# Kernel tuning notes

Hardware: AMD Instinct MI355X
Metric: run time of the kernel (lower is better)

Reference implementation:

```python
import jax, jax.numpy as jnp
import numpy as np

K, PS, WS, WT = 7, 7, 8, 1
NHEADS, STRIDE0, STRIDE1 = 2, 4, 1


def reflect(idx, n):
    # mirror (no edge repeat) reflection, as in stnls reflect_bounds
    idx = jnp.where(idx < 0, -idx, idx)
    idx = jnp.where(idx >= n, 2 * (n - 1) - idx, idx)
    return idx


def setup_inputs():
    key = jax.random.key(0)
    k0, k1 = jax.random.split(key)
    B, T, C, H, W = 1, 4, 64, 192, 192
    vid0 = jax.random.normal(k0, (B, T, C, H, W), jnp.float32)
    vid1 = jax.random.normal(k1, (B, T, C, H, W), jnp.float32)
    return {"vid0": vid0, "vid1": vid1}


def _search(vid0, vid1):
    B, T, C, H, W = vid0.shape
    m = NHEADS
    cph = C // m
    psh = PS // 2
    nH, nW = H // STRIDE0, W // STRIDE0
    qh = jnp.arange(nH) * STRIDE0  # query centers (stride0 grid)
    qw = jnp.arange(nW) * STRIDE0
    dy = jnp.arange(PS) - psh  # patch offsets
    h0 = reflect(qh[:, None] + dy[None, :], H)  # [nH, ps]
    w0 = reflect(qw[:, None] + dy[None, :], W)  # [nW, ps]
    # query patches: [B,T,m,cph,nH,nW,ps,ps]
    P0 = vid0[:, :, :, h0[:, None, :, None], w0[None, :, None, :]]
    P0 = P0.reshape(B, T, m, cph, nH, nW, PS, PS)

    wsh = (WS - 1) // 2
    doff = (jnp.arange(WS) - wsh) * STRIDE1  # spatial window offsets
    dts = jnp.arange(-WT, WT + 1)  # temporal window offsets
    DT, DI, DJ = jnp.meshgrid(dts, doff, doff, indexing="ij")
    offs = jnp.stack([DT.ravel(), DI.ravel(), DJ.ravel()], -1)  # [L,3]
    tbase = jnp.arange(T)

    def one_offset(off):
        dt, di, dj = off[0], off[1], off[2]
        tmap = jnp.clip(tbase + dt, 0, T - 1)  # clamp temporal window
        h1 = reflect(qh[:, None] + di + dy[None, :], H)
        w1 = reflect(qw[:, None] + dj + dy[None, :], W)
        P1 = vid1[:, tmap][:, :, :, h1[:, None, :, None], w1[None, :, None, :]]
        P1 = P1.reshape(B, T, m, cph, nH, nW, PS, PS)
        # per-head product distance (inner product over patch)
        return jnp.einsum("btmchwyx,btmchwyx->btmhw", P0, P1)

    dists_all = jax.lax.map(one_offset, offs)  # [L,B,T,m,nH,nW]
    L = offs.shape[0]
    Q = T * nH * nW
    dists_all = jnp.transpose(dists_all, (1, 3, 2, 4, 5, 0)).reshape(B, m, Q, L)
    vals, idx = jax.lax.top_k(dists_all, K)  # prod search: descending

    # candidate center coordinates per (offset, query axis)
    tc = jnp.clip(tbase[None, :] + offs[:, 0:1], 0, T - 1)  # [L,T]
    hc = reflect(qh[None, :] + offs[:, 1:2], H)  # [L,nH]
    wc = reflect(qw[None, :] + offs[:, 2:3], W)  # [L,nW]
    idxr = idx.reshape(B, m, T, nH, nW, K)
    tsel = tc[idxr, tbase[None, None, :, None, None, None]]
    hsel = hc[idxr, jnp.arange(nH)[None, None, None, :, None, None]]
    wsel = wc[idxr, jnp.arange(nW)[None, None, None, None, :, None]]
    inds = jnp.stack([tsel, hsel, wsel], -1).reshape(B, m, Q, K, 3)
    return vals, inds.astype(jnp.int32)


def reference(vid0, vid1):
    # returns (dists [B,nheads,Q,k], inds [B,nheads,Q,k,3])
    return _search(vid0, vid1)
```

## Files before the change

kernel.cpp:

```cpp
#include <hip/hip_runtime.h>


#define HH 192
#define WW 192
#define HW (HH * WW)
#define TSLICE (192 * 192 * 64)
#define ROWST  (192 * 64)
#define TVID   (4 * TSLICE)

__device__ __forceinline__ int reflect_i(int idx, int n) {
    idx = idx < 0 ? -idx : idx;
    idx = idx >= n ? 2 * (n - 1) - idx : idx;
    return idx;
}

template <int CTRL>
__device__ __forceinline__ float dpp_add(float x) {
    int y = __builtin_amdgcn_update_dpp(0, __float_as_int(x), CTRL, 0xf, 0xf, true);
    return x + __int_as_float(y);
}

__device__ __forceinline__ float reduce32(float v) {
    v = dpp_add<0x111>(v);
    v = dpp_add<0x112>(v);
    v = dpp_add<0x114>(v);
    v = dpp_add<0x118>(v);
    v = dpp_add<0x142>(v);
    return v;
}

__global__ __launch_bounds__(256) void transpose_k(
    const float* __restrict__ v0, const float* __restrict__ v1,
    float* __restrict__ ws)
{
    __shared__ float tile[64 * 65];
    const int wt  = blockIdx.x;
    const int h   = blockIdx.y;
    const int z   = blockIdx.z;
    const int vid = z >> 2;
    const int t   = z & 3;
    const int w0  = wt * 64;
    const int tid = threadIdx.x;
    const int a   = tid & 63;
    const int g   = tid >> 6;
    const float* src = (vid ? v1 : v0) + (size_t)t * 64 * HW + h * WW + w0;
    float* dst = ws + (size_t)vid * TVID + ((size_t)(t * 192 + h) * 192 + w0) * 64;
    #pragma unroll
    for (int cc = g; cc < 64; cc += 4)
        tile[cc * 65 + a] = src[(size_t)cc * HW + a];
    __syncthreads();
    #pragma unroll
    for (int ww = g; ww < 64; ww += 4)
        dst[ww * 64 + a] = tile[a * 65 + ww];
}

__global__ __launch_bounds__(256) void nls_fast(
    const float* __restrict__ T0,
    const float* __restrict__ T1,
    float* __restrict__ out)
{
    __shared__ float score[2 * 192];

    const int b    = blockIdx.x;
    const int xcd  = b & 7;
    const int loc  = b >> 3;
    const int qjp  = loc % 24;
    const int r1   = loc / 24;
    const int qi_l = r1 % 6;
    const int r2   = r1 / 6;
    const int t    = r2 & 3;
    const int hd   = r2 >> 2;
    const int qi   = xcd * 6 + qi_l;

    const int qh  = qi * 4;
    const int qw0 = qjp * 8;

    const int tid  = threadIdx.x;
    const int lane = tid & 63;
    const int wid  = tid >> 6;

    const int c     = lane & 31;
    const int hhalf = lane >> 5;
    const int q     = wid >> 1;
    const int d     = wid & 1;
    const int cg    = hd * 32 + c;
    const int qwq   = qw0 + 4 * q;

    float a[7][7];
    {
        #pragma unroll
        for (int y = 0; y < 7; ++y) {
            const int hv = reflect_i(qh - 3 + y, HH);
            const float* rp = T0 + (size_t)(t * 192 + hv) * ROWST + cg;
            #pragma unroll
            for (int x = 0; x < 7; ++x) {
                const int wv = reflect_i(qwq - 3 + x, WW);
                a[y][x] = rp[wv * 64];
            }
        }
    }

    const bool interior = (qi >= 2) && (qi <= 46) && (qjp >= 1) && (qjp <= 22);

#define FMA_BLOCK(RWBUF)                                                 \
    {                                                                    \
        const int dlo = r > 6 ? r - 6 : 0;                               \
        const int dhi = r < 3 ? r : 3;                                   \
        _Pragma("unroll")                                                \
        for (int dip = 0; dip < 4; ++dip) {                              \
            if (dip >= dlo && dip <= dhi) {                              \
                const int y = r - dip;                                   \
                _Pragma("unroll")                                        \
                for (int djp = 0; djp < 4; ++djp) {                      \
                    _Pragma("unroll")                                    \
                    for (int x = 0; x < 7; ++x) {                        \
                        acc[dip * 4 + djp] =                             \
                            fmaf(a[y][x], (RWBUF)[djp + x], acc[dip * 4 + djp]); \
                    }                                                    \
                }                                                        \
            }                                                            \
        }                                                                \
    }

    float acc[16];
    int tprev = -1;
    #pragma unroll 1
    for (int dtI = 0; dtI < 3; ++dtI) {
        int tp = t + dtI - 1;
        tp = tp < 0 ? 0 : (tp > 3 ? 3 : tp);

        if (tp != tprev) {
            tprev = tp;
            #pragma unroll
            for (int k = 0; k < 16; ++k) acc[k] = 0.f;

            float rwb[3][10];

            if (interior) {
                const float* P = T1 + (size_t)(tp * 192 + qh - 6 + 4 * d) * ROWST
                               + (qwq - 6 + 4 * hhalf) * 64 + cg;
                #pragma unroll
                for (int v = 0; v < 10; ++v) rwb[0][v] = P[v * 64];
                #pragma unroll
                for (int v = 0; v < 10; ++v) rwb[1][v] = P[ROWST + v * 64];
                #pragma unroll
                for (int r = 0; r < 10; ++r) {
                    if (r + 2 < 10) {
                        const float* pr = P + (size_t)(r + 2) * ROWST;
                        #pragma unroll
                        for (int v = 0; v < 10; ++v)
                            rwb[(r + 2) % 3][v] = pr[v * 64];
                    }
                    FMA_BLOCK(rwb[r % 3])
                }
            } else {
                int wo[10];
                #pragma unroll
                for (int v = 0; v < 10; ++v)
                    wo[v] = reflect_i(qwq - 6 + 4 * hhalf + v, WW) * 64 + cg;
                const float* Pt = T1 + (size_t)tp * TSLICE;
                {
                    const float* pr0 = Pt + (size_t)reflect_i(qh - 6 + 4 * d, HH) * ROWST;
                    const float* pr1 = Pt + (size_t)reflect_i(qh - 5 + 4 * d, HH) * ROWST;
                    #pragma unroll
                    for (int v = 0; v < 10; ++v) rwb[0][v] = pr0[wo[v]];
                    #pragma unroll
                    for (int v = 0; v < 10; ++v) rwb[1][v] = pr1[wo[v]];
                }
                #pragma unroll
                for (int r = 0; r < 10; ++r) {
                    if (r + 2 < 10) {
                        const int hv = reflect_i(qh - 6 + 4 * d + r + 2, HH);
                        const float* pr = Pt + (size_t)hv * ROWST;
                        #pragma unroll
                        for (int v = 0; v < 10; ++v)
                            rwb[(r + 2) % 3][v] = pr[wo[v]];
                    }
                    FMA_BLOCK(rwb[r % 3])
                }
            }

            #pragma unroll
            for (int k = 0; k < 16; ++k) acc[k] = reduce32(acc[k]);
        }

        if ((lane & 31) == 31) {
            float* sp = &score[q * 192 + dtI * 64 + 4 * hhalf];
            #pragma unroll
            for (int dip = 0; dip < 4; ++dip)
                #pragma unroll
                for (int djp = 0; djp < 4; ++djp)
                    sp[(4 * d + dip) * 8 + djp] = acc[dip * 4 + djp];
        }
    }
#undef FMA_BLOCK

    __syncthreads();

    if (wid < 2) {
        const int qq = wid;
        const int qj = 2 * qjp + qq;
        float v0 = score[qq * 192 + lane];
        float v1 = score[qq * 192 + 64 + lane];
        float v2 = score[qq * 192 + 128 + lane];
        const int qglob = (t * 48 + qi) * 48 + qj;
        const int vbase = (hd * 9216 + qglob) * 7;
        const int ibase = 129024 + vbase * 3;
        for (int r = 0; r < 7; ++r) {
            float bv = v0; int bi = lane;
            if (v1 > bv) { bv = v1; bi = lane + 64; }
            if (v2 > bv) { bv = v2; bi = lane + 128; }
            #pragma unroll
            for (int m = 1; m <= 32; m <<= 1) {
                float ov = __shfl_xor(bv, m);
                int   oi = __shfl_xor(bi, m);
                if (ov > bv || (ov == bv && oi < bi)) { bv = ov; bi = oi; }
            }
            if (lane == 0) {
                out[vbase + r] = bv;
                int dtSel = bi >> 6;
                int rr    = bi & 63;
                int diSel = (rr >> 3) - 3;
                int djSel = (rr & 7) - 3;
                int ts = t + dtSel - 1;
                ts = ts < 0 ? 0 : (ts > 3 ? 3 : ts);
                int hs = reflect_i(qh + diSel, HH);
                int ws = reflect_i(qj * 4 + djSel, WW);
                float* op = out + ibase + 3 * r;
                op[0] = (float)ts;
                op[1] = (float)hs;
                op[2] = (float)ws;
            }
            if ((bi & 63) == lane) {
                int slot = bi >> 6;
                if (slot == 0)      v0 = -3.4e38f;
                else if (slot == 1) v1 = -3.4e38f;
                else                v2 = -3.4e38f;
            }
        }
    }
}

#define BS_CSTR 282
#define BS_SZ   (32 * BS_CSTR)
#define AF_CSTR 86

__global__ __launch_bounds__(256) void nls_kernel(
    const float* __restrict__ vid0,
    const float* __restrict__ vid1,
    float* __restrict__ out)
{
    __shared__ float smem[BS_SZ + 2 * 192];
    float* Bs = smem;
    float* Asf = smem;
    float* score = smem + BS_SZ;

    const int b    = blockIdx.x;
    const int xcd  = b & 7;
    const int loc  = b >> 3;
    const int qjp  = loc % 24;
    const int r1   = loc / 24;
    const int qi_l = r1 % 6;
    const int r2   = r1 / 6;
    const int t    = r2 & 3;
    const int hd   = r2 >> 2;
    const int qi   = xcd * 6 + qi_l;

    const int qh  = qi * 4;
    const int qw0 = qjp * 8;

    const int tid  = threadIdx.x;
    const int lane = tid & 63;
    const int wid  = tid >> 6;

    const bool intA = (qi >= 1) && (qjp >= 1) && (qjp <= 22);
    const bool intB = (qi >= 2) && (qi <= 46) && (qjp >= 1) && (qjp <= 22);

    if (intA) {
        const int sc = tid & 31;
        const int gg = tid >> 5;
        const float* src = vid0 + (size_t)(t * 64 + hd * 32 + sc) * HW
                         + (qh - 3) * WW + (qw0 - 3);
        float* dstc = Asf + sc * AF_CSTR;
        for (int it = gg; it < 21; it += 8) {
            int u = it / 3, grp = it - u * 3;
            float4 val = *(const float4*)(src + u * WW + 4 * grp);
            float* dp = dstc + u * 12 + 4 * grp;
            *(float2*)(dp)     = make_float2(val.x, val.y);
            *(float2*)(dp + 2) = make_float2(val.z, val.w);
        }
    } else {
        const int sc = tid >> 3;
        const int vl = tid & 7;
        const float* src = vid0 + (size_t)(t * 64 + hd * 32 + sc) * HW;
        const int wa0 = reflect_i(qw0 - 3 + vl, WW);
        const int wa1 = (vl < 4) ? reflect_i(qw0 + 5 + vl, WW) : 0;
        float* dst = Asf + sc * AF_CSTR + vl;
        #pragma unroll
        for (int u = 0; u < 7; ++u) {
            int hh = reflect_i(qh - 3 + u, HH);
            const float* rp = src + hh * WW;
            dst[u * 12] = rp[wa0];
            if (vl < 4) dst[u * 12 + 8] = rp[wa1];
        }
    }
    __syncthreads();

    const int c     = lane & 31;
    const int hhalf = lane >> 5;
    const int q     = wid >> 1;
    const int d     = wid & 1;

    float a[7][8];
    {
        const float* Ab = Asf + c * AF_CSTR + 4 * q;
        #pragma unroll
        for (int y = 0; y < 7; ++y) {
            #pragma unroll
            for (int j = 0; j < 4; ++j)
                *(float2*)&a[y][2 * j] = *(const float2*)(Ab + y * 12 + 2 * j);
        }
    }

    const float* Bc = Bs + c * BS_CSTR + (4 * d) * 20 + 4 * q + 4 * hhalf;

    int tprev = -1;
    #pragma unroll 1
    for (int dtI = 0; dtI < 3; ++dtI) {
        int tp = t + dtI - 1;
        tp = tp < 0 ? 0 : (tp > 3 ? 3 : tp);
        __syncthreads();
        if (tp == tprev) {
            if (tid < 128) {
                int qq = tid >> 6, o = tid & 63;
                score[qq * 192 + dtI * 64 + o] = score[qq * 192 + (dtI - 1) * 64 + o];
            }
            continue;
        }
        tprev = tp;

        if (intB) {
            const int sc = tid & 31;
            const int gg = tid >> 5;
            const float* src = vid1 + (size_t)(tp * 64 + hd * 32 + sc) * HW
                             + (qh - 6) * WW + (qw0 - 6);
            float* dstc = Bs + sc * BS_CSTR;
            for (int it = gg; it < 70; it += 8) {
                int u = it / 5, grp = it - u * 5;
                float4 val = *(const float4*)(src + u * WW + 4 * grp);
                float* dp = dstc + u * 20 + 4 * grp;
                *(float2*)(dp)     = make_float2(val.x, val.y);
                *(float2*)(dp + 2) = make_float2(val.z, val.w);
            }
        } else {
            const int sc = tid >> 3;
            const int vl = tid & 7;
            const float* src = vid1 + (size_t)(tp * 64 + hd * 32 + sc) * HW;
            const int w0 = reflect_i(qw0 - 6 + vl, WW);
            const int w1 = reflect_i(qw0 + 2 + vl, WW);
            const int w2 = (vl < 4) ? reflect_i(qw0 + 10 + vl, WW) : 0;
            float* dst = Bs + sc * BS_CSTR + vl;
            #pragma unroll
            for (int u = 0; u < 14; ++u) {
                int hh2 = reflect_i(qh - 6 + u, HH);
                const float* rp = src + hh2 * WW;
                dst[u * 20]     = rp[w0];
                dst[u * 20 + 8] = rp[w1];
                if (vl < 4) dst[u * 20 + 16] = rp[w2];
            }
        }
        __syncthreads();

        {
            float acc[16];
            #pragma unroll
            for (int k = 0; k < 16; ++k) acc[k] = 0.f;
            #pragma unroll
            for (int r = 0; r < 10; ++r) {
                float rw[12];
                const float* Br = Bc + r * 20;
                #pragma unroll
                for (int j = 0; j < 6; ++j)
                    *(float2*)&rw[2 * j] = *(const float2*)(Br + 2 * j);
                const int dlo = r > 6 ? r - 6 : 0;
                const int dhi = r < 3 ? r : 3;
                #pragma unroll
                for (int dip = 0; dip < 4; ++dip) {
                    if (dip >= dlo && dip <= dhi) {
                        const int y = r - dip;
                        #pragma unroll
                        for (int djp = 0; djp < 4; ++djp)
                            #pragma unroll
                            for (int x = 0; x < 7; ++x)
                                acc[dip * 4 + djp] =
                                    fmaf(a[y][x], rw[djp + x], acc[dip * 4 + djp]);
                    }
                }
            }
            #pragma unroll
            for (int k = 0; k < 16; ++k) acc[k] = reduce32(acc[k]);
            if ((lane & 31) == 31) {
                float* sp = &score[q * 192 + dtI * 64 + 4 * hhalf];
                #pragma unroll
                for (int dip = 0; dip < 4; ++dip) {
                    float* dp = sp + (4 * d + dip) * 8;
                    *(float2*)(dp)     = make_float2(acc[dip * 4 + 0], acc[dip * 4 + 1]);
                    *(float2*)(dp + 2) = make_float2(acc[dip * 4 + 2], acc[dip * 4 + 3]);
                }
            }
        }
    }

    __syncthreads();

    if (wid < 2) {
        const int qq = wid;
        const int qj = 2 * qjp + qq;
        float v0 = score[qq * 192 + lane];
        float v1 = score[qq * 192 + 64 + lane];
        float v2 = score[qq * 192 + 128 + lane];
        const int qglob = (t * 48 + qi) * 48 + qj;
        const int vbase = (hd * 9216 + qglob) * 7;
        const int ibase = 129024 + vbase * 3;
        for (int r = 0; r < 7; ++r) {
            float bv = v0; int bi = lane;
            if (v1 > bv) { bv = v1; bi = lane + 64; }
            if (v2 > bv) { bv = v2; bi = lane + 128; }
            #pragma unroll
            for (int m = 1; m <= 32; m <<= 1) {
                float ov = __shfl_xor(bv, m);
                int   oi = __shfl_xor(bi, m);
                if (ov > bv || (ov == bv && oi < bi)) { bv = ov; bi = oi; }
            }
            if (lane == 0) {
                out[vbase + r] = bv;
                int dtSel = bi >> 6;
                int rr    = bi & 63;
                int diSel = (rr >> 3) - 3;
                int djSel = (rr & 7) - 3;
                int ts = t + dtSel - 1;
                ts = ts < 0 ? 0 : (ts > 3 ? 3 : ts);
                int hs = reflect_i(qh + diSel, HH);
                int ws = reflect_i(qj * 4 + djSel, WW);
                float* op = out + ibase + 3 * r;
                op[0] = (float)ts;
                op[1] = (float)hs;
                op[2] = (float)ws;
            }
            if ((bi & 63) == lane) {
                int slot = bi >> 6;
                if (slot == 0)      v0 = -3.4e38f;
                else if (slot == 1) v1 = -3.4e38f;
                else                v2 = -3.4e38f;
            }
        }
    }
}

extern "C" void kernel_launch(void* const* d_in, const int* in_sizes, int n_in,
                              void* d_out, int out_size, void* d_ws, size_t ws_size,
                              hipStream_t stream) {
    const float* vid0 = (const float*)d_in[0];
    const float* vid1 = (const float*)d_in[1];
    float* out = (float*)d_out;
    const size_t need = 2ull * (size_t)TVID * sizeof(float);
    if (ws_size >= need) {
        float* ws = (float*)d_ws;
        transpose_k<<<dim3(3, 192, 8), 256, 0, stream>>>(vid0, vid1, ws);
        nls_fast<<<dim3(9216), 256, 0, stream>>>(ws, ws + TVID, out);
    } else {
        nls_kernel<<<dim3(9216), 256, 0, stream>>>(vid0, vid1, out);
    }
}
```

Before: 330.4 us.

## Replace per-accumulator wave reductions with butterfly merge-reduce and cross-slice row prefetch

```diff
diff --git a/kernel.cpp b/kernel.cpp
--- a/kernel.cpp
+++ b/kernel.cpp
@@ -17,6 +17,12 @@
 template <int CTRL>
 __device__ __forceinline__ float dpp_add(float x) {
     int y = __builtin_amdgcn_update_dpp(0, __float_as_int(x), CTRL, 0xf, 0xf, true);
+    return x + __int_as_float(y);
+}
+
+template <int PAT>
+__device__ __forceinline__ float swz_add(float x) {
+    int y = __builtin_amdgcn_ds_swizzle(__float_as_int(x), PAT);
     return x + __int_as_float(y);
 }
 
@@ -27,6 +33,35 @@
     v = dpp_add<0x118>(v);
     v = dpp_add<0x142>(v);
     return v;
+}
+
+__device__ __forceinline__ float merge_reduce(const float* acc,
+                                              bool b0, bool b1, bool b2, bool b3) {
+    float u[8];
+    #pragma unroll
+    for (int j = 0; j < 8; ++j) {
+        float e = dpp_add<0xB1>(acc[2 * j]);
+        float o = dpp_add<0xB1>(acc[2 * j + 1]);
+        u[j] = b0 ? o : e;
+    }
+    float v[4];
+    #pragma unroll
+    for (int i = 0; i < 4; ++i) {
+        float e = dpp_add<0x4E>(u[2 * i]);
+        float o = dpp_add<0x4E>(u[2 * i + 1]);
+        v[i] = b1 ? o : e;
+    }
+    float w[2];
+    #pragma unroll
+    for (int m = 0; m < 2; ++m) {
+        float e = swz_add<0x101F>(v[2 * m]);
+        float o = swz_add<0x101F>(v[2 * m + 1]);
+        w[m] = b2 ? o : e;
+    }
+    float s0 = swz_add<0x201F>(w[0]);
+    float s1 = swz_add<0x201F>(w[1]);
+    float S  = b3 ? s1 : s0;
+    return swz_add<0x401F>(S);
 }
 
 __global__ __launch_bounds__(256) void transpose_k(
@@ -86,6 +121,14 @@
     const int cg    = hd * 32 + c;
     const int qwq   = qw0 + 4 * q;
 
+    const bool b0 = (lane & 1) != 0;
+    const bool b1 = (lane & 2) != 0;
+    const bool b2 = (lane & 4) != 0;
+    const bool b3 = (lane & 8) != 0;
+    const bool writer = (lane & 16) == 0;
+    const int  kL   = lane & 15;
+    const int  svoff = q * 192 + (4 * d + (kL >> 2)) * 8 + 4 * hhalf + (kL & 3);
+
     float a[7][7];
     {
         #pragma unroll
@@ -101,6 +144,11 @@
     }
 
     const bool interior = (qi >= 2) && (qi <= 46) && (qjp >= 1) && (qjp <= 22);
+
+    int wo[10];
+    #pragma unroll
+    for (int v = 0; v < 10; ++v)
+        wo[v] = reflect_i(qwq - 6 + 4 * hhalf + v, WW) * 64 + cg;
 
 #define FMA_BLOCK(RWBUF)                                                 \
     {                                                                    \
@@ -114,15 +162,35 @@
                 for (int djp = 0; djp < 4; ++djp) {                      \
                     _Pragma("unroll")                                    \
                     for (int x = 0; x < 7; ++x) {                        \
-                        acc[dip * 4 + djp] =                             \
-                            fmaf(a[y][x], (RWBUF)[djp + x], acc[dip * 4 + djp]); \
+                        if (y == 0 && x == 0)                            \
+                            acc[dip * 4 + djp] = a[0][0] * (RWBUF)[djp]; \
+                        else                                             \
+                            acc[dip * 4 + djp] =                         \
+                                fmaf(a[y][x], (RWBUF)[djp + x], acc[dip * 4 + djp]); \
                     }                                                    \
                 }                                                        \
             }                                                            \
         }                                                                \
     }
 
+    float rwb[2][10];
     float acc[16];
+    float S = 0.f;
+
+    const int tp0 = (t > 0) ? t - 1 : 0;
+
+    if (interior) {
+        const float* P0 = T1 + (size_t)(tp0 * 192 + qh - 6 + 4 * d) * ROWST
+                        + (qwq - 6 + 4 * hhalf) * 64 + cg;
+        #pragma unroll
+        for (int v = 0; v < 10; ++v) rwb[0][v] = P0[v * 64];
+    } else {
+        const int hv0 = reflect_i(qh - 6 + 4 * d, HH);
+        const float* pr = T1 + (size_t)tp0 * TSLICE + (size_t)hv0 * ROWST;
+        #pragma unroll
+        for (int v = 0; v < 10; ++v) rwb[0][v] = pr[wo[v]];
+    }
+
     int tprev = -1;
     #pragma unroll 1
     for (int dtI = 0; dtI < 3; ++dtI) {
@@ -131,67 +199,39 @@
 
         if (tp != tprev) {
             tprev = tp;
-            #pragma unroll
-            for (int k = 0; k < 16; ++k) acc[k] = 0.f;
-
-            float rwb[3][10];
 
             if (interior) {
                 const float* P = T1 + (size_t)(tp * 192 + qh - 6 + 4 * d) * ROWST
                                + (qwq - 6 + 4 * hhalf) * 64 + cg;
-                #pragma unroll
-                for (int v = 0; v < 10; ++v) rwb[0][v] = P[v * 64];
-                #pragma unroll
-                for (int v = 0; v < 10; ++v) rwb[1][v] = P[ROWST + v * 64];
+                const float* Pn0 = P + (tp < 3 ? TSLICE : 0);
                 #pragma unroll
                 for (int r = 0; r < 10; ++r) {
-                    if (r + 2 < 10) {
-                        const float* pr = P + (size_t)(r + 2) * ROWST;
-                        #pragma unroll
-                        for (int v = 0; v < 10; ++v)
-                            rwb[(r + 2) % 3][v] = pr[v * 64];
-                    }
-                    FMA_BLOCK(rwb[r % 3])
+                    const float* nrp = (r < 9) ? (P + (size_t)(r + 1) * ROWST) : Pn0;
+                    #pragma unroll
+                    for (int v = 0; v < 10; ++v)
+                        rwb[(r + 1) & 1][v] = nrp[v * 64];
+                    FMA_BLOCK(rwb[r & 1])
                 }
             } else {
-                int wo[10];
-                #pragma unroll
-                for (int v = 0; v < 10; ++v)
-                    wo[v] = reflect_i(qwq - 6 + 4 * hhalf + v, WW) * 64 + cg;
-                const float* Pt = T1 + (size_t)tp * TSLICE;
-                {
-                    const float* pr0 = Pt + (size_t)reflect_i(qh - 6 + 4 * d, HH) * ROWST;
-                    const float* pr1 = Pt + (size_t)reflect_i(qh - 5 + 4 * d, HH) * ROWST;
-                    #pragma unroll
-                    for (int v = 0; v < 10; ++v) rwb[0][v] = pr0[wo[v]];
-                    #pragma unroll
-                    for (int v = 0; v < 10; ++v) rwb[1][v] = pr1[wo[v]];
-                }
+                const float* Ptb = T1 + (size_t)tp * TSLICE;
+                const float* Ptn = (tp < 3) ? (Ptb + TSLICE) : Ptb;
                 #pragma unroll
                 for (int r = 0; r < 10; ++r) {
-                    if (r + 2 < 10) {
-                        const int hv = reflect_i(qh - 6 + 4 * d + r + 2, HH);
-                        const float* pr = Pt + (size_t)hv * ROWST;
-                        #pragma unroll
-                        for (int v = 0; v < 10; ++v)
-                            rwb[(r + 2) % 3][v] = pr[wo[v]];
-                    }
-                    FMA_BLOCK(rwb[r % 3])
+                    const int nr = (r < 9) ? r + 1 : 0;
+                    const float* nb = (r < 9) ? Ptb : Ptn;
+                    const int hv = reflect_i(qh - 6 + 4 * d + nr, HH);
+                    const float* pr = nb + (size_t)hv * ROWST;
+                    #pragma unroll
+                    for (int v = 0; v < 10; ++v)
+                        rwb[(r + 1) & 1][v] = pr[wo[v]];
+                    FMA_BLOCK(rwb[r & 1])
                 }
             }
 
-            #pragma unroll
-            for (int k = 0; k < 16; ++k) acc[k] = reduce32(acc[k]);
-        }
-
-        if ((lane & 31) == 31) {
-            float* sp = &score[q * 192 + dtI * 64 + 4 * hhalf];
-            #pragma unroll
-            for (int dip = 0; dip < 4; ++dip)
-                #pragma unroll
-                for (int djp = 0; djp < 4; ++djp)
-                    sp[(4 * d + dip) * 8 + djp] = acc[dip * 4 + djp];
-        }
+            S = merge_reduce(acc, b0, b1, b2, b3);
+        }
+
+        if (writer) score[svoff + dtI * 64] = S;
     }
 #undef FMA_BLOCK
 
```

After: 321.3 us. 1.03x faster.
